# Kernel tuning notes

Measured on AMD Instinct MI355X. Metric: run time of the kernel, lower is better.

Reference implementation:

```python
import jax, jax.numpy as jnp
import numpy as np

D_MODEL = 1024
HEADS = 16
D_K = D_MODEL // HEADS
SCALE = 1.0 / np.sqrt(D_K)


def setup_inputs() -> dict:
    key = jax.random.key(0)
    ks = jax.random.split(key, 12)
    B, S = 4, 2048
    std = 1.0 / np.sqrt(D_MODEL)
    inp = {
        "query": jax.random.normal(ks[0], (B, S, D_MODEL), jnp.float32),
        "key": jax.random.normal(ks[1], (B, S, D_MODEL), jnp.float32),
        "value": jax.random.normal(ks[2], (B, S, D_MODEL), jnp.float32),
        # projection weights stored [in, out] (transpose of torch Linear)
        "Wq": jax.random.normal(ks[3], (D_MODEL, D_MODEL), jnp.float32) * std,
        "bq": jax.random.normal(ks[4], (D_MODEL,), jnp.float32) * std,
        "Wk": jax.random.normal(ks[5], (D_MODEL, D_MODEL), jnp.float32) * std,
        "bk": jax.random.normal(ks[6], (D_MODEL,), jnp.float32) * std,
        "Wv": jax.random.normal(ks[7], (D_MODEL, D_MODEL), jnp.float32) * std,
        "bv": jax.random.normal(ks[8], (D_MODEL,), jnp.float32) * std,
        "Wo": jax.random.normal(ks[9], (D_MODEL, D_MODEL), jnp.float32) * std,
        "bo": jax.random.normal(ks[10], (D_MODEL,), jnp.float32) * std,
    }
    return inp


def _proj(x, W, b):
    # [B,S,D] -> [B,S,H,Dk]
    B, S, _ = x.shape
    return (x @ W + b).reshape(B, S, HEADS, D_K)


def reference(query, key, value, Wq, bq, Wk, bk, Wv, bv, Wo, bo):
    B, S, _ = query.shape
    Q = _proj(query, Wq, bq)
    K = _proj(key, Wk, bk)
    V = _proj(value, Wv, bv)
    scores = jnp.einsum('bihd,bjhd->bijh', Q, K) * SCALE
    # FAITHFUL to original: nn.Softmax(dim=1) normalizes over the QUERY axis i
    attn = jax.nn.softmax(scores, axis=1)
    # dropout is identity at inference
    x = jnp.einsum('bijh,bjhd->bihd', attn, V).reshape(B, S, D_MODEL)
    return x @ Wo + bo
```

## Files before the change

### kernel.cpp

```cpp
#include <hip/hip_runtime.h>


#define B_   4
#define S_   2048
#define D_   1024
#define H_   16
#define DK_  64
#define BH_  64
#define SCALE_  0.125f
#define SC2_    0.18033688f
#define ECL_    72.134f

typedef __bf16 bf16x2 __attribute__((ext_vector_type(2)));
typedef __bf16 bf16x4 __attribute__((ext_vector_type(4)));
typedef __bf16 bf16x8 __attribute__((ext_vector_type(8)));
typedef float  f32x4  __attribute__((ext_vector_type(4)));
typedef unsigned int u32;

#define MFMA16(a,b,c) __builtin_amdgcn_mfma_f32_16x16x32_bf16((a),(b),(c),0,0,0)

__device__ __forceinline__ bf16x8 ld8(const __bf16* p){ return *(const bf16x8*)p; }

__device__ __forceinline__ void gll16(const __bf16* g, __bf16* l) {
    __builtin_amdgcn_global_load_lds(
        (const __attribute__((address_space(1))) u32*)g,
        (__attribute__((address_space(3))) u32*)l, 16, 0, 0);
}

__global__ __launch_bounds__(256) void wtrans3(
    const float* __restrict__ W0, const float* __restrict__ W1,
    const float* __restrict__ W2, __bf16* __restrict__ Wt)
{
    __shared__ __align__(16) __bf16 Ls[64][80];
    const int t = threadIdx.x;
    const int k0 = blockIdx.x * 64, n0 = blockIdx.y * 64, z = blockIdx.z;
    const float* W = (z == 0) ? W0 : ((z == 1) ? W1 : W2);
    __bf16* out = Wt + (size_t)z * D_ * D_;

#pragma unroll
    for (int p = 0; p < 4; ++p) {
        int id = p*256 + t;
        int k = id >> 4, nq = id & 15;
        f32x4 v = *(const f32x4*)&W[(size_t)(k0 + k)*D_ + n0 + nq*4];
#pragma unroll
        for (int u = 0; u < 4; ++u) Ls[nq*4 + u][k] = (__bf16)v[u];
    }
    __syncthreads();
#pragma unroll
    for (int p = 0; p < 2; ++p) {
        int id = p*256 + t;
        int n = id >> 3, c = id & 7;
        *(bf16x8*)&out[(size_t)(n0 + n)*D_ + k0 + c*8] =
            *(const bf16x8*)&Ls[n][c*8];
    }
}

template<int ABF16, int MODE>
__global__ __launch_bounds__(256) void gemm128(
    const void* __restrict__ Ap, const __bf16* __restrict__ Wt,
    const float* __restrict__ bias, void* __restrict__ C)
{
    __shared__ __align__(16) __bf16 As[128*32];
    __shared__ __align__(16) __bf16 Bs[128*32];

    const int t = threadIdx.x, lane = t & 63, w = t >> 6;
    const int wm = w >> 1, wn = w & 1;
    const int fr = lane & 15, fq = lane >> 4;
    const int m0 = blockIdx.y * 128, n0 = blockIdx.x * 128;

    f32x4 acc[4][4];
#pragma unroll
    for (int i = 0; i < 4; ++i)
#pragma unroll
        for (int j = 0; j < 4; ++j) acc[i][j] = (f32x4){0.f,0.f,0.f,0.f};

    for (int kk = 0; kk < D_; kk += 32) {
        __syncthreads();
        if (ABF16) {
            const __bf16* Ab = (const __bf16*)Ap;
#pragma unroll
            for (int p = 0; p < 2; ++p) {
                int c = p*256 + t;
                int row = c >> 2, l = (c & 3) ^ (row & 3);
                gll16(&Ab[(size_t)(m0 + row)*D_ + kk + l*8],
                      &As[(size_t)(p*256 + (t & ~63))*8]);
            }
        } else {
            const float* Af = (const float*)Ap;
#pragma unroll
            for (int p = 0; p < 2; ++p) {
                int c = p*256 + t;
                int row = c >> 2, ch = c & 3;
                const float* ap = &Af[(size_t)(m0 + row)*D_ + kk + ch*8];
                f32x4 x0 = *(const f32x4*)ap;
                f32x4 x1 = *(const f32x4*)(ap + 4);
                bf16x8 v = { (__bf16)x0[0], (__bf16)x0[1], (__bf16)x0[2], (__bf16)x0[3],
                             (__bf16)x1[0], (__bf16)x1[1], (__bf16)x1[2], (__bf16)x1[3] };
                *(bf16x8*)&As[row*32 + 8*(ch ^ (row & 3))] = v;
            }
        }
#pragma unroll
        for (int p = 0; p < 2; ++p) {
            int c = p*256 + t;
            int n = c >> 2, l = (c & 3) ^ (n & 3);
            gll16(&Wt[(size_t)(n0 + n)*D_ + kk + l*8],
                  &Bs[(size_t)(p*256 + (t & ~63))*8]);
        }
        __syncthreads();

        bf16x8 af[4], bfr[4];
#pragma unroll
        for (int mt = 0; mt < 4; ++mt) {
            int row = wm*64 + mt*16 + fr;
            af[mt] = ld8(&As[row*32 + 8*(fq ^ (row & 3))]);
        }
#pragma unroll
        for (int nt = 0; nt < 4; ++nt) {
            int n = wn*64 + nt*16 + fr;
            bfr[nt] = ld8(&Bs[n*32 + 8*(fq ^ (n & 3))]);
        }
#pragma unroll
        for (int mt = 0; mt < 4; ++mt)
#pragma unroll
            for (int nt = 0; nt < 4; ++nt)
                acc[mt][nt] = MFMA16(af[mt], bfr[nt], acc[mt][nt]);
    }

#pragma unroll
    for (int mt = 0; mt < 4; ++mt)
#pragma unroll
        for (int nt = 0; nt < 4; ++nt) {
            int colg = n0 + wn*64 + nt*16 + fr;
            float bv = bias[colg];
#pragma unroll
            for (int r = 0; r < 4; ++r) {
                int rowg = m0 + wm*64 + mt*16 + fq*4 + r;
                float o = acc[mt][nt][r] + bv;
                if (MODE == 0) {
                    ((float*)C)[(size_t)rowg*D_ + colg] = o;
                } else {
                    int b = rowg >> 11, sp = rowg & (S_-1);
                    int h = colg >> 6, dk = colg & 63;
                    ((__bf16*)C)[(((size_t)(b*H_ + h))*S_ + sp)*DK_ + dk] = (__bf16)o;
                }
            }
        }
}

__global__ __launch_bounds__(256) void colsum_rcp(
    const __bf16* __restrict__ Q, const __bf16* __restrict__ K,
    float* __restrict__ Rl)
{
    __shared__ __align__(16) __bf16 Qs[2][64*64];
    const int t = threadIdx.x, lane = t & 63, w = t >> 6;
    const int fr = lane & 15, fq = lane >> 4;
    const int bh = blockIdx.y;
    const int jw = blockIdx.x*256 + w*64;
    const __bf16* Qb = Q + (size_t)bh*S_*DK_;
    const __bf16* Kb = K + (size_t)bh*S_*DK_;

    bf16x8 kh[4][2];
#pragma unroll
    for (int jt = 0; jt < 4; ++jt) {
        const __bf16* kr = &Kb[(size_t)(jw + jt*16 + fr)*DK_];
        kh[jt][0] = ld8(kr + fq*8);
        kh[jt][1] = ld8(kr + 32 + fq*8);
    }

    float accl[4][4] = {};

#pragma unroll
    for (int p = 0; p < 2; ++p) {
        int c = p*256 + t;
        int i = c >> 3, l = (c & 7) ^ (i & 7);
        gll16(&Qb[(size_t)i*DK_ + l*8], &Qs[0][(size_t)(p*256 + (t & ~63))*8]);
    }
    __syncthreads();

    for (int i0 = 0; i0 < S_; i0 += 64) {
        const int cur = (i0 >> 6) & 1;
        if (i0 + 64 < S_) {
#pragma unroll
            for (int p = 0; p < 2; ++p) {
                int c = p*256 + t;
                int i = c >> 3, l = (c & 7) ^ (i & 7);
                gll16(&Qb[(size_t)(i0 + 64 + i)*DK_ + l*8],
                      &Qs[cur ^ 1][(size_t)(p*256 + (t & ~63))*8]);
            }
        }
#pragma unroll
        for (int it = 0; it < 4; ++it) {
            int i = it*16 + fr;
            bf16x8 q0 = ld8(&Qs[cur][i*64 + 8*(fq ^ (i & 7))]);
            bf16x8 q1 = ld8(&Qs[cur][i*64 + 8*((4 + fq) ^ (i & 7))]);
#pragma unroll
            for (int jt = 0; jt < 4; ++jt) {
                f32x4 s = MFMA16(kh[jt][0], q0, ((f32x4){0.f,0.f,0.f,0.f}));
                s = MFMA16(kh[jt][1], q1, s);
#pragma unroll
                for (int r = 0; r < 4; ++r)
                    accl[jt][r] += __builtin_amdgcn_exp2f(
                                       fminf(s[r]*SC2_, ECL_));
            }
        }
        __syncthreads();
    }
#pragma unroll
    for (int jt = 0; jt < 4; ++jt)
#pragma unroll
        for (int r = 0; r < 4; ++r) {
            accl[jt][r] += __shfl_xor(accl[jt][r], 1, 64);
            accl[jt][r] += __shfl_xor(accl[jt][r], 2, 64);
            accl[jt][r] += __shfl_xor(accl[jt][r], 4, 64);
            accl[jt][r] += __shfl_xor(accl[jt][r], 8, 64);
        }
    if (fr == 0) {
#pragma unroll
        for (int jt = 0; jt < 4; ++jt)
#pragma unroll
            for (int r = 0; r < 4; ++r)
                Rl[(size_t)bh*S_ + jw + jt*16 + fq*4 + r] = 1.0f / accl[jt][r];
    }
}

__global__ __launch_bounds__(512, 4) void attn_pv(
    const __bf16* __restrict__ Q, const __bf16* __restrict__ K,
    const __bf16* __restrict__ V, const float* __restrict__ Rl,
    __bf16* __restrict__ X)
{
    __shared__ __align__(16) __bf16 Ks[2][64*64];
    __shared__ __align__(16) __bf16 Vs[2][64*64];
    __shared__ __align__(16) __bf16 Pl[8][32*64];

    const int t = threadIdx.x, lane = t & 63, w = t >> 6;
    const int fr = lane & 15, fq = lane >> 4;
    const int bh = blockIdx.y;
    const int iw = blockIdx.x*256 + w*32;
    const __bf16* Qb = Q + (size_t)bh*S_*DK_;
    const __bf16* Kb = K + (size_t)bh*S_*DK_;
    const __bf16* Vb = V + (size_t)bh*S_*DK_;
    const float*  Rb = Rl + (size_t)bh*S_;

    bf16x8 qf[2][2];
#pragma unroll
    for (int it = 0; it < 2; ++it)
#pragma unroll
        for (int kf = 0; kf < 2; ++kf)
            qf[it][kf] = ld8(&Qb[(size_t)(iw + it*16 + fr)*DK_ + kf*32 + fq*8]);

    const int dq = t & 15, jp = t >> 4;
    const int krow = t >> 3;
    const int kchk = (t & 7) ^ (krow & 7);

    f32x4 acc[2][4];
#pragma unroll
    for (int it = 0; it < 2; ++it)
#pragma unroll
        for (int dt = 0; dt < 4; ++dt) acc[it][dt] = (f32x4){0.f,0.f,0.f,0.f};

    gll16(&Kb[(size_t)krow*DK_ + kchk*8], &Ks[0][(t & ~63)*8]);
    __syncthreads();

    for (int jg = 0; jg < S_; jg += 64) {
        const int cur = (jg >> 6) & 1;

        bf16x4 v0 = *(const bf16x4*)&Vb[(size_t)(jg + 2*jp    )*DK_ + dq*4];
        bf16x4 v1 = *(const bf16x4*)&Vb[(size_t)(jg + 2*jp + 1)*DK_ + dq*4];
        f32x4 rl[4];
#pragma unroll
        for (int jt = 0; jt < 4; ++jt)
            rl[jt] = *(const f32x4*)&Rb[jg + jt*16 + fq*4];
        if (jg + 64 < S_)
            gll16(&Kb[(size_t)(jg + 64 + krow)*DK_ + kchk*8],
                  &Ks[cur ^ 1][(t & ~63)*8]);

#pragma unroll
        for (int jt = 0; jt < 4; ++jt) {
            const __bf16* kb = &Ks[cur][(jt*16 + fr)*64];
            bf16x8 af0 = ld8(kb + ((fq    ) ^ (fr & 7))*8);
            bf16x8 af1 = ld8(kb + ((fq + 4) ^ (fr & 7))*8);
#pragma unroll
            for (int it = 0; it < 2; ++it) {
                f32x4 s = MFMA16(af0, qf[it][0], ((f32x4){0.f,0.f,0.f,0.f}));
                s = MFMA16(af1, qf[it][1], s);
                bf16x4 pv;
#pragma unroll
                for (int r = 0; r < 4; ++r)
                    pv[r] = (__bf16)(__builtin_amdgcn_exp2f(
                                fminf(s[r]*SC2_, ECL_)) * rl[jt][r]);
                int il = it*16 + fr;
                *(bf16x4*)&Pl[w][il*64 + (((jt*4 + fq) ^ (2*(fr & 7))))*4] = pv;
            }
        }

#pragma unroll
        for (int u = 0; u < 4; ++u) {
            int d = dq*4 + u;
            int f = (d ^ dq) & 7;
            *(bf16x2*)&Vs[cur][d*64 + (((jp >> 2) ^ f))*8 + (jp & 3)*2] =
                (bf16x2){ v0[u], v1[u] };
        }
        __syncthreads();

#pragma unroll
        for (int kh = 0; kh < 2; ++kh) {
            bf16x8 pa0 = ld8(&Pl[w][(     fr)*64 + (((fq + 4*kh) ^ (fr & 7)))*8]);
            bf16x8 pa1 = ld8(&Pl[w][(16 + fr)*64 + (((fq + 4*kh) ^ (fr & 7)))*8]);
#pragma unroll
            for (int dt = 0; dt < 4; ++dt) {
                int d = dt*16 + fr;
                int f = (d ^ (d >> 2)) & 7;
                bf16x8 vb = ld8(&Vs[cur][d*64 + (((kh*4 + fq) ^ f))*8]);
                acc[0][dt] = MFMA16(pa0, vb, acc[0][dt]);
                acc[1][dt] = MFMA16(pa1, vb, acc[1][dt]);
            }
        }
    }

    const int b = bh >> 4, h = bh & 15;
#pragma unroll
    for (int it = 0; it < 2; ++it)
#pragma unroll
        for (int dt = 0; dt < 4; ++dt)
#pragma unroll
            for (int r = 0; r < 4; ++r) {
                int i = iw + it*16 + fq*4 + r;
                X[((size_t)b*S_ + i)*D_ + h*DK_ + dt*16 + fr] =
                    (__bf16)acc[it][dt][r];
            }
}

extern "C" void kernel_launch(void* const* d_in, const int* in_sizes, int n_in,
                              void* d_out, int out_size, void* d_ws, size_t ws_size,
                              hipStream_t stream)
{
    const float* query = (const float*)d_in[0];
    const float* key   = (const float*)d_in[1];
    const float* value = (const float*)d_in[2];
    const float* Wq = (const float*)d_in[3];  const float* bq = (const float*)d_in[4];
    const float* Wk = (const float*)d_in[5];  const float* bk = (const float*)d_in[6];
    const float* Wv = (const float*)d_in[7];  const float* bv = (const float*)d_in[8];
    const float* Wo = (const float*)d_in[9];  const float* bo = (const float*)d_in[10];

    char* ws = (char*)d_ws;
    char* dob = (char*)d_out;
    const size_t MiB = 1024 * 1024;
    __bf16* Qb = (__bf16*)(ws);
    __bf16* Kb = (__bf16*)(ws + 16 * MiB);
    __bf16* Vb = (__bf16*)(ws + 32 * MiB);
    __bf16* Xb = (__bf16*)(ws + 48 * MiB);
    float*  Rlb = (float*)d_out;
    __bf16* Wt3 = (__bf16*)(dob + 1 * MiB);
    __bf16* WtO = (__bf16*)(ws);

    wtrans3<<<dim3(16,16,3), 256, 0, stream>>>(Wq, Wk, Wv, Wt3);

    dim3 gg(D_/128, (B_*S_)/128);
    gemm128<0,1><<<gg, 256, 0, stream>>>(query, Wt3,              bq, Qb);
    gemm128<0,1><<<gg, 256, 0, stream>>>(key,   Wt3 + (size_t)D_*D_,   bk, Kb);
    gemm128<0,1><<<gg, 256, 0, stream>>>(value, Wt3 + (size_t)2*D_*D_, bv, Vb);

    colsum_rcp<<<dim3(S_/256, BH_), 256, 0, stream>>>(Qb, Kb, Rlb);

    attn_pv<<<dim3(S_/256, BH_), 512, 0, stream>>>(Qb, Kb, Vb, Rlb, Xb);

    wtrans3<<<dim3(16,16,1), 256, 0, stream>>>(Wo, Wo, Wo, WtO);

    gemm128<1,0><<<gg, 256, 0, stream>>>(Xb, WtO, bo, d_out);
}
```

Measured before the change: 460.6 us.

## Fold softmax scale into Q projection, drop clamp, remap grids for L2 locality

Multiplies the Q projection output by the log2e-scaled softmax factor inside the GEMM epilogue, so the colsum and PV kernels call exp2 directly on the scores and skip the per-element multiply and clamp. The GEMM and attention grids become 1D with the row-block or head index as the fast dimension, which changes the order blocks are scheduled in and aims at better cache reuse. colsum_rcp now handles 32 columns per wave instead of 64, doubling its grid to add parallelism. Removing the overflow clamp and quantising the pre-scaled Q to bf16 risk overflow and a small accuracy change.

```diff
diff --git a/kernel.cpp b/kernel.cpp
--- a/kernel.cpp
+++ b/kernel.cpp
@@ -7,9 +7,7 @@
 #define H_   16
 #define DK_  64
 #define BH_  64
-#define SCALE_  0.125f
 #define SC2_    0.18033688f
-#define ECL_    72.134f
 
 typedef __bf16 bf16x2 __attribute__((ext_vector_type(2)));
 typedef __bf16 bf16x4 __attribute__((ext_vector_type(4)));
@@ -55,7 +53,7 @@
     }
 }
 
-template<int ABF16, int MODE>
+template<int ABF16, int MODE, int QS>
 __global__ __launch_bounds__(256) void gemm128(
     const void* __restrict__ Ap, const __bf16* __restrict__ Wt,
     const float* __restrict__ bias, void* __restrict__ C)
@@ -66,7 +64,8 @@
     const int t = threadIdx.x, lane = t & 63, w = t >> 6;
     const int wm = w >> 1, wn = w & 1;
     const int fr = lane & 15, fq = lane >> 4;
-    const int m0 = blockIdx.y * 128, n0 = blockIdx.x * 128;
+    const int gid = blockIdx.x;
+    const int m0 = (gid & 63) * 128, n0 = (gid >> 6) * 128;
 
     f32x4 acc[4][4];
 #pragma unroll
@@ -136,6 +135,7 @@
             for (int r = 0; r < 4; ++r) {
                 int rowg = m0 + wm*64 + mt*16 + fq*4 + r;
                 float o = acc[mt][nt][r] + bv;
+                if (QS) o *= SC2_;
                 if (MODE == 0) {
                     ((float*)C)[(size_t)rowg*D_ + colg] = o;
                 } else {
@@ -154,20 +154,21 @@
     __shared__ __align__(16) __bf16 Qs[2][64*64];
     const int t = threadIdx.x, lane = t & 63, w = t >> 6;
     const int fr = lane & 15, fq = lane >> 4;
-    const int bh = blockIdx.y;
-    const int jw = blockIdx.x*256 + w*64;
+    const int gid = blockIdx.x;
+    const int bh = gid & 63;
+    const int jw = (gid >> 6)*128 + w*32;
     const __bf16* Qb = Q + (size_t)bh*S_*DK_;
     const __bf16* Kb = K + (size_t)bh*S_*DK_;
 
-    bf16x8 kh[4][2];
-#pragma unroll
-    for (int jt = 0; jt < 4; ++jt) {
+    bf16x8 kh[2][2];
+#pragma unroll
+    for (int jt = 0; jt < 2; ++jt) {
         const __bf16* kr = &Kb[(size_t)(jw + jt*16 + fr)*DK_];
         kh[jt][0] = ld8(kr + fq*8);
         kh[jt][1] = ld8(kr + 32 + fq*8);
     }
 
-    float accl[4][4] = {};
+    float accl[2][4] = {};
 
 #pragma unroll
     for (int p = 0; p < 2; ++p) {
@@ -194,19 +195,18 @@
             bf16x8 q0 = ld8(&Qs[cur][i*64 + 8*(fq ^ (i & 7))]);
             bf16x8 q1 = ld8(&Qs[cur][i*64 + 8*((4 + fq) ^ (i & 7))]);
 #pragma unroll
-            for (int jt = 0; jt < 4; ++jt) {
+            for (int jt = 0; jt < 2; ++jt) {
                 f32x4 s = MFMA16(kh[jt][0], q0, ((f32x4){0.f,0.f,0.f,0.f}));
                 s = MFMA16(kh[jt][1], q1, s);
 #pragma unroll
                 for (int r = 0; r < 4; ++r)
-                    accl[jt][r] += __builtin_amdgcn_exp2f(
-                                       fminf(s[r]*SC2_, ECL_));
+                    accl[jt][r] += __builtin_amdgcn_exp2f(s[r]);
             }
         }
         __syncthreads();
     }
 #pragma unroll
-    for (int jt = 0; jt < 4; ++jt)
+    for (int jt = 0; jt < 2; ++jt)
 #pragma unroll
         for (int r = 0; r < 4; ++r) {
             accl[jt][r] += __shfl_xor(accl[jt][r], 1, 64);
@@ -216,7 +216,7 @@
         }
     if (fr == 0) {
 #pragma unroll
-        for (int jt = 0; jt < 4; ++jt)
+        for (int jt = 0; jt < 2; ++jt)
 #pragma unroll
             for (int r = 0; r < 4; ++r)
                 Rl[(size_t)bh*S_ + jw + jt*16 + fq*4 + r] = 1.0f / accl[jt][r];
@@ -234,8 +234,9 @@
 
     const int t = threadIdx.x, lane = t & 63, w = t >> 6;
     const int fr = lane & 15, fq = lane >> 4;
-    const int bh = blockIdx.y;
-    const int iw = blockIdx.x*256 + w*32;
+    const int gid = blockIdx.x;
+    const int bh = gid & 63;
+    const int iw = (gid >> 6)*256 + w*32;
     const __bf16* Qb = Q + (size_t)bh*S_*DK_;
     const __bf16* Kb = K + (size_t)bh*S_*DK_;
     const __bf16* Vb = V + (size_t)bh*S_*DK_;
@@ -286,8 +287,7 @@
                 bf16x4 pv;
 #pragma unroll
                 for (int r = 0; r < 4; ++r)
-                    pv[r] = (__bf16)(__builtin_amdgcn_exp2f(
-                                fminf(s[r]*SC2_, ECL_)) * rl[jt][r]);
+                    pv[r] = (__bf16)(__builtin_amdgcn_exp2f(s[r]) * rl[jt][r]);
                 int il = it*16 + fr;
                 *(bf16x4*)&Pl[w][il*64 + (((jt*4 + fq) ^ (2*(fr & 7))))*4] = pv;
             }
@@ -355,16 +355,15 @@
 
     wtrans3<<<dim3(16,16,3), 256, 0, stream>>>(Wq, Wk, Wv, Wt3);
 
-    dim3 gg(D_/128, (B_*S_)/128);
-    gemm128<0,1><<<gg, 256, 0, stream>>>(query, Wt3,              bq, Qb);
-    gemm128<0,1><<<gg, 256, 0, stream>>>(key,   Wt3 + (size_t)D_*D_,   bk, Kb);
-    gemm128<0,1><<<gg, 256, 0, stream>>>(value, Wt3 + (size_t)2*D_*D_, bv, Vb);
-
-    colsum_rcp<<<dim3(S_/256, BH_), 256, 0, stream>>>(Qb, Kb, Rlb);
-
-    attn_pv<<<dim3(S_/256, BH_), 512, 0, stream>>>(Qb, Kb, Vb, Rlb, Xb);
+    gemm128<0,1,1><<<512, 256, 0, stream>>>(query, Wt3,                  bq, Qb);
+    gemm128<0,1,0><<<512, 256, 0, stream>>>(key,   Wt3 + (size_t)D_*D_,  bk, Kb);
+    gemm128<0,1,0><<<512, 256, 0, stream>>>(value, Wt3 + (size_t)2*D_*D_,bv, Vb);
+
+    colsum_rcp<<<1024, 256, 0, stream>>>(Qb, Kb, Rlb);
+
+    attn_pv<<<512, 512, 0, stream>>>(Qb, Kb, Vb, Rlb, Xb);
 
     wtrans3<<<dim3(16,16,1), 256, 0, stream>>>(Wo, Wo, Wo, WtO);
 
-    gemm128<1,0><<<gg, 256, 0, stream>>>(Xb, WtO, bo, d_out);
-}
+    gemm128<1,0,0><<<512, 256, 0, stream>>>(Xb, WtO, bo, d_out);
+}
```

After: 425.4 us. -7.7%, faster.
